# Optimization experiments

Hardware: AMD Instinct MI355X
Metric: run time of the kernel (lower is better)

Reference implementation:

```python
import jax, jax.numpy as jnp
import numpy as np

B, T, D = 2, 2048, 1024
H = 16
HD = D // H
EPS = 1e-6


def rmsnorm(x, w):
    # x: [..., HD]
    var = jnp.mean(x * x, axis=-1, keepdims=True)
    return x * jax.lax.rsqrt(var + EPS) * w


def setup_inputs() -> dict:
    key = jax.random.key(0)
    ks = jax.random.split(key, 12)
    s = 1.0 / np.sqrt(D)
    return {
        "query": jax.random.normal(ks[0], (B, T, D), jnp.float32),
        "key_value": jax.random.normal(ks[1], (B, T, D), jnp.float32),
        "Wq": jax.random.normal(ks[2], (D, D), jnp.float32) * s,
        "bq": jnp.zeros((D,), jnp.float32),
        "Wk": jax.random.normal(ks[3], (D, D), jnp.float32) * s,
        "bk": jnp.zeros((D,), jnp.float32),
        "Wv": jax.random.normal(ks[4], (D, D), jnp.float32) * s,
        "bv": jnp.zeros((D,), jnp.float32),
        "Wo": jax.random.normal(ks[5], (D, D), jnp.float32) * s,
        "bo": jnp.zeros((D,), jnp.float32),
        "qn_w": jnp.ones((HD,), jnp.float32),
        "kn_w": jnp.ones((HD,), jnp.float32),
    }


def reference(query, key_value, Wq, bq, Wk, bk, Wv, bv, Wo, bo, qn_w, kn_w):
    scale = HD ** -0.5
    # projections -> [B, H, T, HD]
    def split_heads(x):
        return x.reshape(B, T, H, HD).transpose(0, 2, 1, 3)
    q = split_heads(query @ Wq.T + bq)
    k = split_heads(key_value @ Wk.T + bk)
    v = split_heads(key_value @ Wv.T + bv)
    q = rmsnorm(q, qn_w)
    k = rmsnorm(k, kn_w)
    attn = jnp.einsum('bhqd,bhkd->bhqk', q, k) * scale  # [B,H,T,T]
    attn = jax.nn.softmax(attn, axis=-1)
    out = jnp.einsum('bhqk,bhkd->bhqd', attn, v)
    out = out.transpose(0, 2, 1, 3).reshape(B, T, D)
    return out @ Wo.T + bo
```

## Files before the change

### kernel.cpp

```cpp
#include <hip/hip_runtime.h>
#include <stdint.h>

#define Bb 2
#define Tt 2048
#define Dd 1024
#define Hh 16
#define HDd 64
#define Mm 4096

typedef __attribute__((ext_vector_type(4))) float f32x4;
typedef __attribute__((ext_vector_type(8))) __bf16 bf16x8;
typedef __attribute__((ext_vector_type(8))) short s16x8;
typedef __attribute__((ext_vector_type(4))) short s16x4;
typedef __attribute__((ext_vector_type(4))) float fvec4;
typedef __attribute__((ext_vector_type(4))) unsigned int u32x4;

__device__ __forceinline__ float bf2f(ushort u){
  union { unsigned int i; float f; } v; v.i = ((unsigned int)u) << 16; return v.f;
}
__device__ __forceinline__ ushort f2bf(float f){
  union { float f; unsigned int i; } v; v.f = f;
  unsigned int u = v.i;
  u += 0x7FFFu + ((u >> 16) & 1u);
  return (ushort)(u >> 16);
}

__device__ __forceinline__ void gload16(const void* g, void* l){
  __builtin_amdgcn_global_load_lds(
      (const __attribute__((address_space(1))) void*)g,
      (__attribute__((address_space(3))) void*)l, 16, 0, 0);
}

__device__ __forceinline__ bf16x8 cat4(s16x4 a, s16x4 b){
  s16x8 c = __builtin_shufflevector(a, b, 0,1,2,3,4,5,6,7);
  return __builtin_bit_cast(bf16x8, c);
}

__global__ __launch_bounds__(256) void cvt_all(
    const float* __restrict__ q, const float* __restrict__ kv,
    const float* __restrict__ wq, const float* __restrict__ wk,
    const float* __restrict__ wv, const float* __restrict__ wo,
    ushort* __restrict__ oq, ushort* __restrict__ okv, ushort* __restrict__ owq,
    ushort* __restrict__ owk, ushort* __restrict__ owv, ushort* __restrict__ owo)
{
  const int NQ = Mm*Dd/4;
  const int NW = Dd*Dd/4;
  int j = blockIdx.x * 256 + threadIdx.x;
  const float* s; ushort* d;
  if (j < NQ)            { s = q;  d = oq;  }
  else if ((j -= NQ) < NQ){ s = kv; d = okv; }
  else if ((j -= NQ) < NW){ s = wq; d = owq; }
  else if ((j -= NW) < NW){ s = wk; d = owk; }
  else if ((j -= NW) < NW){ s = wv; d = owv; }
  else        { j -= NW;   s = wo; d = owo; }
  fvec4 v = ((const fvec4*)s)[j];
  unsigned int lo = (unsigned int)f2bf(v.x) | ((unsigned int)f2bf(v.y) << 16);
  unsigned int hi = (unsigned int)f2bf(v.z) | ((unsigned int)f2bf(v.w) << 16);
  ((uint2*)d)[j] = make_uint2(lo, hi);
}

template<int MODE>
__device__ __forceinline__ void gemm_body(
    const ushort* __restrict__ A, const ushort* __restrict__ W,
    const float* __restrict__ bias, ushort* __restrict__ Oh, float* __restrict__ Of,
    const float* __restrict__ nw, float rmsScale,
    int m0, int n0, int N, int K)
{
  __shared__ ushort As[128*64];
  __shared__ ushort Bs[128*64];
  const int tid  = threadIdx.x;
  const int w    = tid >> 6, lid = tid & 63;
  const int lrow = lid & 15, g = lid >> 4;
  const int wm   = (w >> 1) << 6, wn = (w & 1) << 6;

  f32x4 acc[4][4] = {};

  for (int kt = 0; kt < K; kt += 64){
    __syncthreads();
    #pragma unroll
    for (int i = 0; i < 4; ++i){
      int e   = tid + i*256;
      int row = e >> 3;
      int c   = (e & 7) ^ (row & 7);
      gload16(A + (size_t)(m0 + row)*K + kt + c*8, &As[e*8]);
      gload16(W + (size_t)(n0 + row)*K + kt + c*8, &Bs[e*8]);
    }
    __syncthreads();
    #pragma unroll
    for (int kc = 0; kc < 2; ++kc){
      bf16x8 af[4], bfr[4];
      #pragma unroll
      for (int r = 0; r < 4; ++r){
        int row = wm + r*16 + lrow;
        af[r] = *(const bf16x8*)&As[row*64 + (((kc*4 + g) ^ (row & 7)) << 3)];
      }
      #pragma unroll
      for (int c = 0; c < 4; ++c){
        int row = wn + c*16 + lrow;
        bfr[c] = *(const bf16x8*)&Bs[row*64 + (((kc*4 + g) ^ (row & 7)) << 3)];
      }
      #pragma unroll
      for (int r = 0; r < 4; ++r)
        #pragma unroll
        for (int c = 0; c < 4; ++c)
          acc[r][c] = __builtin_amdgcn_mfma_f32_16x16x32_bf16(af[r], bfr[c], acc[r][c], 0, 0, 0);
    }
  }
  const int colbase = n0 + wn;
  float bv[4], wv4[4];
  #pragma unroll
  for (int c = 0; c < 4; ++c){
    bv[c] = bias[colbase + c*16 + lrow];
    if (MODE == 1) wv4[c] = nw[c*16 + lrow];
  }
  #pragma unroll
  for (int r = 0; r < 4; ++r){
    #pragma unroll
    for (int b = 0; b < 4; ++b){
      float v[4];
      #pragma unroll
      for (int c = 0; c < 4; ++c) v[c] = acc[r][c][b] + bv[c];
      float sc = 1.0f;
      if (MODE == 1){
        float ss = v[0]*v[0] + v[1]*v[1] + v[2]*v[2] + v[3]*v[3];
        ss += __shfl_xor(ss, 1, 64);
        ss += __shfl_xor(ss, 2, 64);
        ss += __shfl_xor(ss, 4, 64);
        ss += __shfl_xor(ss, 8, 64);
        sc = rsqrtf(ss * (1.0f/64.0f) + 1e-6f) * rmsScale;
      }
      int row = m0 + wm + r*16 + g*4 + b;
      #pragma unroll
      for (int c = 0; c < 4; ++c){
        int col = colbase + c*16 + lrow;
        if (MODE == 2)      Of[(size_t)row*N + col] = v[c];
        else if (MODE == 1) Oh[(size_t)row*N + col] = f2bf(v[c] * sc * wv4[c]);
        else                Oh[(size_t)row*N + col] = f2bf(v[c]);
      }
    }
  }
}

__global__ __launch_bounds__(256) void gemm_qkv(
  const ushort* __restrict__ qbf, const ushort* __restrict__ kvbf,
  const ushort* __restrict__ wq, const ushort* __restrict__ wk, const ushort* __restrict__ wv,
  const float* __restrict__ bq, const float* __restrict__ bk, const float* __restrict__ bv,
  const float* __restrict__ qnw, const float* __restrict__ knw,
  ushort* __restrict__ Q, ushort* __restrict__ Kx, ushort* __restrict__ V)
{
  int bid = blockIdx.x;
  int mt  = bid / 24;
  int ntg = bid % 24;
  int proj = ntg >> 3, nt = ntg & 7;
  if (proj == 0)
    gemm_body<1>(qbf, wq, bq, Q, nullptr, qnw, 0.18033688011112042f, mt*128, nt*128, Dd, Dd);
  else if (proj == 1)
    gemm_body<1>(kvbf, wk, bk, Kx, nullptr, knw, 1.0f, mt*128, nt*128, Dd, Dd);
  else
    gemm_body<0>(kvbf, wv, bv, V, nullptr, nullptr, 1.0f, mt*128, nt*128, Dd, Dd);
}

__global__ __launch_bounds__(256) void gemm_o(
  const ushort* __restrict__ X, const ushort* __restrict__ wo,
  const float* __restrict__ bo, float* __restrict__ out)
{
  int bid = blockIdx.x;
  int mt = bid / 8, nt = bid % 8;
  gemm_body<2>(X, wo, bo, nullptr, out, nullptr, 1.0f, mt*128, nt*128, Dd, Dd);
}

__global__ __launch_bounds__(256, 2) void attn_k(
  const ushort* __restrict__ Qb, const ushort* __restrict__ Kb,
  const ushort* __restrict__ Vb, ushort* __restrict__ Ob)
{
  __shared__ ushort lds[4][64*64];

  const int tid = threadIdx.x;
  const int w   = tid >> 6, lid = tid & 63;
  const int r   = lid & 15, g = lid >> 4;

  int bid = blockIdx.x;
  int wg  = (bid & 7) * 64 + (bid >> 3);
  int bh  = wg >> 4, qt = wg & 15;
  int bb  = bh >> 4, h = bh & 15;
  const size_t base = (size_t)bb * Tt * Dd + (size_t)h * HDd;

  bf16x8 qf[2][2];
  #pragma unroll
  for (int sub = 0; sub < 2; ++sub)
    #pragma unroll
    for (int kc = 0; kc < 2; ++kc)
      qf[sub][kc] = *(const bf16x8*)&Qb[base + (size_t)(qt*128 + w*32 + sub*16 + r)*Dd + kc*32 + g*8];

  const ushort* kfp[2][4];
  #pragma unroll
  for (int kc = 0; kc < 2; ++kc)
    #pragma unroll
    for (int t = 0; t < 4; ++t)
      kfp[kc][t] = &lds[0][(t*16 + r)*64 + (((kc*4 + g) ^ (r & 7)) << 3)];

  const ushort* vfp[4][2][2];
  #pragma unroll
  for (int t16 = 0; t16 < 4; ++t16){
    int d = t16*16 + r, F = ((d >> 3) ^ d) & 7;
    #pragma unroll
    for (int kc = 0; kc < 2; ++kc){
      int c0 = 4*kc + (g >> 1);
      vfp[t16][kc][0] = &lds[2][d*64 + 4*(g & 1) + (((c0    ) ^ F) << 3)];
      vfp[t16][kc][1] = &lds[2][d*64 + 4*(g & 1) + (((c0 + 2) ^ F) << 3)];
    }
  }

  ushort* sca0[8]; ushort* sca1[8];
  #pragma unroll
  for (int i = 0; i < 2; ++i){
    int e = tid + i*256, kr = e >> 3, c8 = (e & 7) << 3;
    #pragma unroll
    for (int j = 0; j < 8; ++j){
      int d = c8 + j, F = ((d >> 3) ^ d) & 7;
      ushort* pp = &lds[2][d*64 + (((kr >> 3) ^ F) << 3) + (kr & 7)];
      if (i == 0) sca0[j] = pp; else sca1[j] = pp;
    }
  }

  ushort* kdst0 = &lds[0][tid*8];
  ushort* kdst1 = &lds[0][(tid + 256)*8];

  const ushort *ks0g, *ks1g, *vs0g, *vs1g;
  {
    int e0 = tid, e1 = tid + 256;
    int r0 = e0 >> 3, c0 = (e0 & 7) ^ (r0 & 7);
    int r1 = e1 >> 3, c1 = (e1 & 7) ^ (r1 & 7);
    ks0g = Kb + base + (size_t)r0 * Dd + c0*8;
    ks1g = Kb + base + (size_t)r1 * Dd + c1*8;
    vs0g = Vb + base + (size_t)(e0 >> 3) * Dd + (e0 & 7)*8;
    vs1g = Vb + base + (size_t)(e1 >> 3) * Dd + (e1 & 7)*8;
  }
  const size_t kstep = (size_t)64 * Dd;

  gload16(ks0g, kdst0);
  gload16(ks1g, kdst1);
  s16x8 vr0 = *(const s16x8*)vs0g;
  s16x8 vr1 = *(const s16x8*)vs1g;
  ks0g += kstep; ks1g += kstep; vs0g += kstep; vs1g += kstep;

  f32x4 o[2][4] = {};
  float mr0 = -1e30f, mr1 = -1e30f;
  float lr0 = 0.f,    lr1 = 0.f;

  auto dosm = [&](const f32x4* s, float& m, float& l, f32x4* oo, bf16x8* pao){
    float t0 = fmaxf(fmaxf(s[0][0], s[0][1]), s[0][2]);
    float t1 = fmaxf(fmaxf(s[0][3], s[1][0]), s[1][1]);
    float t2 = fmaxf(fmaxf(s[1][2], s[1][3]), s[2][0]);
    float t3 = fmaxf(fmaxf(s[2][1], s[2][2]), s[2][3]);
    float t4 = fmaxf(fmaxf(s[3][0], s[3][1]), s[3][2]);
    float mx = fmaxf(fmaxf(fmaxf(t0, t1), fmaxf(t2, t3)), fmaxf(t4, s[3][3]));
    mx = fmaxf(mx, __shfl_xor(mx, 16, 64));
    mx = fmaxf(mx, __shfl_xor(mx, 32, 64));
    const bool defer = (__all(mx - m <= 8.0f) != 0);
    float nm = defer ? m : fmaxf(m, mx);
    float p[4][4]; float rs = 0.f;
    #pragma unroll
    for (int t = 0; t < 4; ++t)
      #pragma unroll
      for (int b = 0; b < 4; ++b){
        float e = __builtin_amdgcn_exp2f(s[t][b] - nm);
        p[t][b] = e; rs += e;
      }
    rs += __shfl_xor(rs, 16, 64);
    rs += __shfl_xor(rs, 32, 64);
    if (defer){
      l += rs;
    } else {
      float f = __builtin_amdgcn_exp2f(m - nm);
      l = l * f + rs; m = nm;
      #pragma unroll
      for (int t16 = 0; t16 < 4; ++t16) oo[t16] *= f;
    }
    #pragma unroll
    for (int kc = 0; kc < 2; ++kc){
      unsigned u0, u1, u2, u3;
      asm("v_cvt_pk_bf16_f32 %0, %1, %2" : "=v"(u0) : "v"(p[2*kc  ][0]), "v"(p[2*kc  ][1]));
      asm("v_cvt_pk_bf16_f32 %0, %1, %2" : "=v"(u1) : "v"(p[2*kc  ][2]), "v"(p[2*kc  ][3]));
      asm("v_cvt_pk_bf16_f32 %0, %1, %2" : "=v"(u2) : "v"(p[2*kc+1][0]), "v"(p[2*kc+1][1]));
      asm("v_cvt_pk_bf16_f32 %0, %1, %2" : "=v"(u3) : "v"(p[2*kc+1][2]), "v"(p[2*kc+1][3]));
      u32x4 uu = {u0, u1, u2, u3};
      pao[kc] = __builtin_bit_cast(bf16x8, uu);
    }
  };

#define ATTN_TILE(BUF, PREFETCH)                                                     \
  {                                                                                  \
    _Pragma("unroll")                                                                \
    for (int j = 0; j < 8; ++j){                                                     \
      *(ushort*)((char*)sca0[j] + (BUF)*8192) = (ushort)vr0[j];                      \
      *(ushort*)((char*)sca1[j] + (BUF)*8192) = (ushort)vr1[j];                      \
    }                                                                                \
    __syncthreads();                                                                 \
    if (PREFETCH){                                                                   \
      gload16(ks0g, (char*)kdst0 + ((BUF)^1)*8192);                                  \
      gload16(ks1g, (char*)kdst1 + ((BUF)^1)*8192);                                  \
      vr0 = *(const s16x8*)vs0g;                                                     \
      vr1 = *(const s16x8*)vs1g;                                                     \
      ks0g += kstep; ks1g += kstep; vs0g += kstep; vs1g += kstep;                    \
    }                                                                                \
    f32x4 s0[4] = {}, s1[4] = {};                                                    \
    __builtin_amdgcn_s_setprio(1);                                                   \
    _Pragma("unroll")                                                                \
    for (int kc = 0; kc < 2; ++kc)                                                   \
      _Pragma("unroll")                                                              \
      for (int t = 0; t < 4; ++t){                                                   \
        bf16x8 kf = *(const bf16x8*)((const char*)kfp[kc][t] + (BUF)*8192);          \
        s0[t] = __builtin_amdgcn_mfma_f32_16x16x32_bf16(kf, qf[0][kc], s0[t], 0,0,0);\
        s1[t] = __builtin_amdgcn_mfma_f32_16x16x32_bf16(kf, qf[1][kc], s1[t], 0,0,0);\
      }                                                                              \
    __builtin_amdgcn_s_setprio(0);                                                   \
    bf16x8 pa0[2], pa1[2];                                                           \
    dosm(s0, mr0, lr0, o[0], pa0);                                                   \
    dosm(s1, mr1, lr1, o[1], pa1);                                                   \
    __builtin_amdgcn_s_setprio(1);                                                   \
    _Pragma("unroll")                                                                \
    for (int t16 = 0; t16 < 4; ++t16){                                               \
      _Pragma("unroll")                                                              \
      for (int kc = 0; kc < 2; ++kc){                                                \
        s16x4 a0 = *(const s16x4*)((const char*)vfp[t16][kc][0] + (BUF)*8192);       \
        s16x4 a1 = *(const s16x4*)((const char*)vfp[t16][kc][1] + (BUF)*8192);       \
        bf16x8 vf = cat4(a0, a1);                                                    \
        o[0][t16] = __builtin_amdgcn_mfma_f32_16x16x32_bf16(vf, pa0[kc], o[0][t16], 0,0,0); \
        o[1][t16] = __builtin_amdgcn_mfma_f32_16x16x32_bf16(vf, pa1[kc], o[1][t16], 0,0,0); \
      }                                                                              \
    }                                                                                \
    __builtin_amdgcn_s_setprio(0);                                                   \
  }

  for (int kt2 = 0; kt2 < 16; ++kt2){
    ATTN_TILE(0, true);
    ATTN_TILE(1, (kt2 != 15));
  }
#undef ATTN_TILE

  #pragma unroll
  for (int sub = 0; sub < 2; ++sub){
    float inv = 1.0f / (sub ? lr1 : lr0);
    int qrow = qt*128 + w*32 + sub*16 + r;
    #pragma unroll
    for (int t16 = 0; t16 < 4; ++t16){
      uint2 u;
      u.x = (unsigned)f2bf(o[sub][t16][0]*inv) | ((unsigned)f2bf(o[sub][t16][1]*inv) << 16);
      u.y = (unsigned)f2bf(o[sub][t16][2]*inv) | ((unsigned)f2bf(o[sub][t16][3]*inv) << 16);
      *(uint2*)&Ob[base + (size_t)qrow*Dd + t16*16 + g*4] = u;
    }
  }
}

extern "C" void kernel_launch(void* const* d_in, const int* in_sizes, int n_in,
                              void* d_out, int out_size, void* d_ws, size_t ws_size,
                              hipStream_t stream)
{
  const float* query = (const float*)d_in[0];
  const float* keyv  = (const float*)d_in[1];
  const float* Wq    = (const float*)d_in[2];
  const float* bq    = (const float*)d_in[3];
  const float* Wk    = (const float*)d_in[4];
  const float* bk    = (const float*)d_in[5];
  const float* Wv    = (const float*)d_in[6];
  const float* bv    = (const float*)d_in[7];
  const float* Wo    = (const float*)d_in[8];
  const float* bo    = (const float*)d_in[9];
  const float* qnw   = (const float*)d_in[10];
  const float* knw   = (const float*)d_in[11];
  float* out = (float*)d_out;

  char* p = (char*)d_ws;
  ushort* qbf  = (ushort*)p; p += (size_t)Mm*Dd*2;
  ushort* kvbf = (ushort*)p; p += (size_t)Mm*Dd*2;
  ushort* wqb  = (ushort*)p; p += (size_t)Dd*Dd*2;
  ushort* wkb  = (ushort*)p; p += (size_t)Dd*Dd*2;
  ushort* wvb  = (ushort*)p; p += (size_t)Dd*Dd*2;
  ushort* wob  = (ushort*)p; p += (size_t)Dd*Dd*2;
  ushort* Qb   = (ushort*)p; p += (size_t)Mm*Dd*2;
  ushort* Kbf  = (ushort*)p; p += (size_t)Mm*Dd*2;
  ushort* Vbf  = (ushort*)p; p += (size_t)Mm*Dd*2;
  ushort* Ab   = (ushort*)p; p += (size_t)Mm*Dd*2;

  cvt_all<<<dim3(12288), dim3(256), 0, stream>>>(query, keyv, Wq, Wk, Wv, Wo,
                                                 qbf, kvbf, wqb, wkb, wvb, wob);

  gemm_qkv<<<dim3(768), dim3(256), 0, stream>>>(qbf, kvbf, wqb, wkb, wvb,
                                                bq, bk, bv, qnw, knw, Qb, Kbf, Vbf);

  attn_k<<<dim3(512), dim3(256), 0, stream>>>(Qb, Kbf, Vbf, Ab);

  gemm_o<<<dim3(256), dim3(256), 0, stream>>>(Ab, wob, bo, out);
}
```

Measured before the change: 141.4 us.

## Split attention KV sequence across two wave groups and merge partial softmax states

The attention block grows to 512 threads. Each half of the waves processes half of the key/value sequence for the same 128 query rows, and the two partial flash-attention states (m, l, O) are merged through LDS at the end. The V transpose scatter is also reworked: each thread packs 4x4 transposed 8-byte chunks instead of issuing 16 scalar stores, so the PV MFMA operand becomes one 16-byte LDS read instead of two 8-byte reads. The aim is more waves per CU for latency hiding and cheaper LDS traffic, at the cost of more LDS (64KB per block), a final merge step, and more register pressure under launch_bounds(512,4).

```diff
diff --git a/kernel.cpp b/kernel.cpp
--- a/kernel.cpp
+++ b/kernel.cpp
@@ -29,11 +29,6 @@
   __builtin_amdgcn_global_load_lds(
       (const __attribute__((address_space(1))) void*)g,
       (__attribute__((address_space(3))) void*)l, 16, 0, 0);
-}
-
-__device__ __forceinline__ bf16x8 cat4(s16x4 a, s16x4 b){
-  s16x8 c = __builtin_shufflevector(a, b, 0,1,2,3,4,5,6,7);
-  return __builtin_bit_cast(bf16x8, c);
 }
 
 __global__ __launch_bounds__(256) void cvt_all(
@@ -169,84 +164,93 @@
   gemm_body<2>(X, wo, bo, nullptr, out, nullptr, 1.0f, mt*128, nt*128, Dd, Dd);
 }
 
-__global__ __launch_bounds__(256, 2) void attn_k(
+__global__ __launch_bounds__(512, 4) void attn_k(
   const ushort* __restrict__ Qb, const ushort* __restrict__ Kb,
   const ushort* __restrict__ Vb, ushort* __restrict__ Ob)
 {
-  __shared__ ushort lds[4][64*64];
-
-  const int tid = threadIdx.x;
-  const int w   = tid >> 6, lid = tid & 63;
-  const int r   = lid & 15, g = lid >> 4;
+  __shared__ ushort lds[8][4096];
+
+  const int tid  = threadIdx.x;
+  const int w    = tid >> 6, lid = tid & 63;
+  const int half = w >> 2,  wq  = w & 3;
+  const int r    = lid & 15, g = lid >> 4;
+  const int e    = tid & 255;
 
   int bid = blockIdx.x;
   int wg  = (bid & 7) * 64 + (bid >> 3);
   int bh  = wg >> 4, qt = wg & 15;
-  int bb  = bh >> 4, h = bh & 15;
-  const size_t base = (size_t)bb * Tt * Dd + (size_t)h * HDd;
+  int bb  = bh >> 4, hh = bh & 15;
+  const size_t base = (size_t)bb * Tt * Dd + (size_t)hh * HDd;
 
   bf16x8 qf[2][2];
   #pragma unroll
   for (int sub = 0; sub < 2; ++sub)
     #pragma unroll
     for (int kc = 0; kc < 2; ++kc)
-      qf[sub][kc] = *(const bf16x8*)&Qb[base + (size_t)(qt*128 + w*32 + sub*16 + r)*Dd + kc*32 + g*8];
-
-  const ushort* kfp[2][4];
+      qf[sub][kc] = *(const bf16x8*)&Qb[base + (size_t)(qt*128 + wq*32 + sub*16 + r)*Dd + kc*32 + g*8];
+
+  ushort* Kl = &lds[4*half][0];
+  ushort* Vl = &lds[4*half + 2][0];
+
+  const char* kfp[2][4];
   #pragma unroll
   for (int kc = 0; kc < 2; ++kc)
     #pragma unroll
     for (int t = 0; t < 4; ++t)
-      kfp[kc][t] = &lds[0][(t*16 + r)*64 + (((kc*4 + g) ^ (r & 7)) << 3)];
-
-  const ushort* vfp[4][2][2];
+      kfp[kc][t] = (const char*)&Kl[(t*16 + r)*64 + (((kc*4 + g) ^ (r & 7)) << 3)];
+
+  const char* vfp[4][2];
   #pragma unroll
   for (int t16 = 0; t16 < 4; ++t16){
     int d = t16*16 + r, F = ((d >> 3) ^ d) & 7;
     #pragma unroll
-    for (int kc = 0; kc < 2; ++kc){
-      int c0 = 4*kc + (g >> 1);
-      vfp[t16][kc][0] = &lds[2][d*64 + 4*(g & 1) + (((c0    ) ^ F) << 3)];
-      vfp[t16][kc][1] = &lds[2][d*64 + 4*(g & 1) + (((c0 + 2) ^ F) << 3)];
-    }
-  }
-
-  ushort* sca0[8]; ushort* sca1[8];
-  #pragma unroll
-  for (int i = 0; i < 2; ++i){
-    int e = tid + i*256, kr = e >> 3, c8 = (e & 7) << 3;
-    #pragma unroll
-    for (int j = 0; j < 8; ++j){
-      int d = c8 + j, F = ((d >> 3) ^ d) & 7;
-      ushort* pp = &lds[2][d*64 + (((kr >> 3) ^ F) << 3) + (kr & 7)];
-      if (i == 0) sca0[j] = pp; else sca1[j] = pp;
-    }
-  }
-
-  ushort* kdst0 = &lds[0][tid*8];
-  ushort* kdst1 = &lds[0][(tid + 256)*8];
-
-  const ushort *ks0g, *ks1g, *vs0g, *vs1g;
+    for (int kc = 0; kc < 2; ++kc)
+      vfp[t16][kc] = (const char*)Vl + d*128 + (((4*kc + g) ^ F) << 4);
+  }
+
+  const int d0 = (e & 15) * 4, key0 = (e >> 4) * 4;
+  char* vsca[4];
   {
-    int e0 = tid, e1 = tid + 256;
-    int r0 = e0 >> 3, c0 = (e0 & 7) ^ (r0 & 7);
-    int r1 = e1 >> 3, c1 = (e1 & 7) ^ (r1 & 7);
-    ks0g = Kb + base + (size_t)r0 * Dd + c0*8;
-    ks1g = Kb + base + (size_t)r1 * Dd + c1*8;
-    vs0g = Vb + base + (size_t)(e0 >> 3) * Dd + (e0 & 7)*8;
-    vs1g = Vb + base + (size_t)(e1 >> 3) * Dd + (e1 & 7)*8;
-  }
+    int chunk = ((key0 >> 5) << 2) | ((key0 & 15) >> 2);
+    int hb    = ((key0 >> 4) & 1) * 8;
+    #pragma unroll
+    for (int dd = 0; dd < 4; ++dd){
+      int row = d0 + dd, F = ((row >> 3) ^ row) & 7;
+      vsca[dd] = (char*)Vl + row*128 + ((chunk ^ F) << 4) + hb;
+    }
+  }
+
+  const int e1 = e + 256;
+  const int kr0 = e >> 3,  kq0 = (e & 7) ^ (kr0 & 7);
+  const int kr1 = e1 >> 3, kq1 = (e1 & 7) ^ (kr1 & 7);
+  const int tb  = half * 1024;
+  const ushort* ksg0 = Kb + base + (size_t)(tb + kr0) * Dd + kq0*8;
+  const ushort* ksg1 = Kb + base + (size_t)(tb + kr1) * Dd + kq1*8;
+  const ushort* vsg  = Vb + base + (size_t)(tb + key0) * Dd + d0;
+  ushort* kd0 = &Kl[e*8];
+  ushort* kd1 = &Kl[e1*8];
   const size_t kstep = (size_t)64 * Dd;
 
-  gload16(ks0g, kdst0);
-  gload16(ks1g, kdst1);
-  s16x8 vr0 = *(const s16x8*)vs0g;
-  s16x8 vr1 = *(const s16x8*)vs1g;
-  ks0g += kstep; ks1g += kstep; vs0g += kstep; vs1g += kstep;
+  gload16(ksg0, kd0);
+  gload16(ksg1, kd1);
+  uint2 vv0 = *(const uint2*)(vsg);
+  uint2 vv1 = *(const uint2*)(vsg + Dd);
+  uint2 vv2 = *(const uint2*)(vsg + 2*Dd);
+  uint2 vv3 = *(const uint2*)(vsg + 3*Dd);
+  ksg0 += kstep; ksg1 += kstep; vsg += kstep;
 
   f32x4 o[2][4] = {};
   float mr0 = -1e30f, mr1 = -1e30f;
   float lr0 = 0.f,    lr1 = 0.f;
+
+  auto vscatter = [&](int bufoff){
+    unsigned x0 = vv0.x, x1 = vv1.x, x2 = vv2.x, x3 = vv3.x;
+    unsigned y0 = vv0.y, y1 = vv1.y, y2 = vv2.y, y3 = vv3.y;
+    *(uint2*)(vsca[0] + bufoff) = make_uint2((x0 & 0xFFFFu) | (x1 << 16), (x2 & 0xFFFFu) | (x3 << 16));
+    *(uint2*)(vsca[1] + bufoff) = make_uint2((x0 >> 16) | (x1 & 0xFFFF0000u), (x2 >> 16) | (x3 & 0xFFFF0000u));
+    *(uint2*)(vsca[2] + bufoff) = make_uint2((y0 & 0xFFFFu) | (y1 << 16), (y2 & 0xFFFFu) | (y3 << 16));
+    *(uint2*)(vsca[3] + bufoff) = make_uint2((y0 >> 16) | (y1 & 0xFFFF0000u), (y2 >> 16) | (y3 & 0xFFFF0000u));
+  };
 
   auto dosm = [&](const f32x4* s, float& m, float& l, f32x4* oo, bf16x8* pao){
     float t0 = fmaxf(fmaxf(s[0][0], s[0][1]), s[0][2]);
@@ -264,8 +268,8 @@
     for (int t = 0; t < 4; ++t)
       #pragma unroll
       for (int b = 0; b < 4; ++b){
-        float e = __builtin_amdgcn_exp2f(s[t][b] - nm);
-        p[t][b] = e; rs += e;
+        float ee = __builtin_amdgcn_exp2f(s[t][b] - nm);
+        p[t][b] = ee; rs += ee;
       }
     rs += __shfl_xor(rs, 16, 64);
     rs += __shfl_xor(rs, 32, 64);
@@ -291,18 +295,16 @@
 
 #define ATTN_TILE(BUF, PREFETCH)                                                     \
   {                                                                                  \
-    _Pragma("unroll")                                                                \
-    for (int j = 0; j < 8; ++j){                                                     \
-      *(ushort*)((char*)sca0[j] + (BUF)*8192) = (ushort)vr0[j];                      \
-      *(ushort*)((char*)sca1[j] + (BUF)*8192) = (ushort)vr1[j];                      \
-    }                                                                                \
+    vscatter((BUF)*8192);                                                            \
     __syncthreads();                                                                 \
     if (PREFETCH){                                                                   \
-      gload16(ks0g, (char*)kdst0 + ((BUF)^1)*8192);                                  \
-      gload16(ks1g, (char*)kdst1 + ((BUF)^1)*8192);                                  \
-      vr0 = *(const s16x8*)vs0g;                                                     \
-      vr1 = *(const s16x8*)vs1g;                                                     \
-      ks0g += kstep; ks1g += kstep; vs0g += kstep; vs1g += kstep;                    \
+      gload16(ksg0, (char*)kd0 + ((BUF)^1)*8192);                                    \
+      gload16(ksg1, (char*)kd1 + ((BUF)^1)*8192);                                    \
+      vv0 = *(const uint2*)(vsg);                                                    \
+      vv1 = *(const uint2*)(vsg + Dd);                                               \
+      vv2 = *(const uint2*)(vsg + 2*Dd);                                             \
+      vv3 = *(const uint2*)(vsg + 3*Dd);                                             \
+      ksg0 += kstep; ksg1 += kstep; vsg += kstep;                                    \
     }                                                                                \
     f32x4 s0[4] = {}, s1[4] = {};                                                    \
     __builtin_amdgcn_s_setprio(1);                                                   \
@@ -310,7 +312,7 @@
     for (int kc = 0; kc < 2; ++kc)                                                   \
       _Pragma("unroll")                                                              \
       for (int t = 0; t < 4; ++t){                                                   \
-        bf16x8 kf = *(const bf16x8*)((const char*)kfp[kc][t] + (BUF)*8192);          \
+        bf16x8 kf = *(const bf16x8*)(kfp[kc][t] + (BUF)*8192);                       \
         s0[t] = __builtin_amdgcn_mfma_f32_16x16x32_bf16(kf, qf[0][kc], s0[t], 0,0,0);\
         s1[t] = __builtin_amdgcn_mfma_f32_16x16x32_bf16(kf, qf[1][kc], s1[t], 0,0,0);\
       }                                                                              \
@@ -323,9 +325,7 @@
     for (int t16 = 0; t16 < 4; ++t16){                                               \
       _Pragma("unroll")                                                              \
       for (int kc = 0; kc < 2; ++kc){                                                \
-        s16x4 a0 = *(const s16x4*)((const char*)vfp[t16][kc][0] + (BUF)*8192);       \
-        s16x4 a1 = *(const s16x4*)((const char*)vfp[t16][kc][1] + (BUF)*8192);       \
-        bf16x8 vf = cat4(a0, a1);                                                    \
+        bf16x8 vf = *(const bf16x8*)(vfp[t16][kc] + (BUF)*8192);                     \
         o[0][t16] = __builtin_amdgcn_mfma_f32_16x16x32_bf16(vf, pa0[kc], o[0][t16], 0,0,0); \
         o[1][t16] = __builtin_amdgcn_mfma_f32_16x16x32_bf16(vf, pa1[kc], o[1][t16], 0,0,0); \
       }                                                                              \
@@ -333,22 +333,46 @@
     __builtin_amdgcn_s_setprio(0);                                                   \
   }
 
-  for (int kt2 = 0; kt2 < 16; ++kt2){
+  for (int kt2 = 0; kt2 < 8; ++kt2){
     ATTN_TILE(0, true);
-    ATTN_TILE(1, (kt2 != 15));
+    ATTN_TILE(1, (kt2 != 7));
   }
 #undef ATTN_TILE
 
-  #pragma unroll
-  for (int sub = 0; sub < 2; ++sub){
-    float inv = 1.0f / (sub ? lr1 : lr0);
-    int qrow = qt*128 + w*32 + sub*16 + r;
-    #pragma unroll
-    for (int t16 = 0; t16 < 4; ++t16){
-      uint2 u;
-      u.x = (unsigned)f2bf(o[sub][t16][0]*inv) | ((unsigned)f2bf(o[sub][t16][1]*inv) << 16);
-      u.y = (unsigned)f2bf(o[sub][t16][2]*inv) | ((unsigned)f2bf(o[sub][t16][3]*inv) << 16);
-      *(uint2*)&Ob[base + (size_t)qrow*Dd + t16*16 + g*4] = u;
+  __syncthreads();
+  float* cbase = (float*)&lds[0][0];
+  if (half == 1){
+    float* pp = cbase + wq*2304 + lid*36;
+    #pragma unroll
+    for (int sub = 0; sub < 2; ++sub)
+      #pragma unroll
+      for (int t16 = 0; t16 < 4; ++t16)
+        *(f32x4*)&pp[(sub*4 + t16)*4] = o[sub][t16];
+    f32x4 ml = {mr0, lr0, mr1, lr1};
+    *(f32x4*)&pp[32] = ml;
+  }
+  __syncthreads();
+  if (half == 0){
+    float* pp = cbase + wq*2304 + lid*36;
+    f32x4 ml = *(const f32x4*)&pp[32];
+    #pragma unroll
+    for (int sub = 0; sub < 2; ++sub){
+      float ms = sub ? mr1 : mr0, ls = sub ? lr1 : lr0;
+      float mp = ml[sub*2], lp = ml[sub*2 + 1];
+      float nm = fmaxf(ms, mp);
+      float es = __builtin_amdgcn_exp2f(ms - nm);
+      float ep = __builtin_amdgcn_exp2f(mp - nm);
+      float inv = 1.0f / (ls*es + lp*ep);
+      int qrow = qt*128 + wq*32 + sub*16 + r;
+      #pragma unroll
+      for (int t16 = 0; t16 < 4; ++t16){
+        f32x4 op = *(const f32x4*)&pp[(sub*4 + t16)*4];
+        f32x4 oc = o[sub][t16]*es + op*ep;
+        uint2 u;
+        u.x = (unsigned)f2bf(oc[0]*inv) | ((unsigned)f2bf(oc[1]*inv) << 16);
+        u.y = (unsigned)f2bf(oc[2]*inv) | ((unsigned)f2bf(oc[3]*inv) << 16);
+        *(uint2*)&Ob[base + (size_t)qrow*Dd + t16*16 + g*4] = u;
+      }
     }
   }
 }
@@ -389,7 +413,7 @@
   gemm_qkv<<<dim3(768), dim3(256), 0, stream>>>(qbf, kvbf, wqb, wkb, wvb,
                                                 bq, bk, bv, qnw, knw, Qb, Kbf, Vbf);
 
-  attn_k<<<dim3(512), dim3(256), 0, stream>>>(Qb, Kbf, Vbf, Ab);
+  attn_k<<<dim3(512), dim3(512), 0, stream>>>(Qb, Kbf, Vbf, Ab);
 
   gemm_o<<<dim3(256), dim3(256), 0, stream>>>(Ab, wob, bo, out);
 }
```

New measurement: 145.5 us. +2.9%, slower.
